# Performance work log

Measured on AMD Instinct MI355X. Metric: run time of the kernel, lower is better.

Reference implementation:

```python
import jax, jax.numpy as jnp
import numpy as np

N_NODES = 1_000_000
N_EDGES = 16_000_000
D = 2          # num_dimensions (hard-coded in source)
H = 64         # hidden_channnels
G = 1024       # number of graphs in the batch


def setup_inputs() -> dict:
    key = jax.random.key(0)
    ks = jax.random.split(key, 10)
    x = jax.random.normal(ks[0], (N_NODES, D), dtype=jnp.float32)
    edge_index = jax.random.randint(ks[1], (2, N_EDGES), 0, N_NODES, dtype=jnp.int64)
    batch = jnp.sort(jax.random.randint(ks[2], (N_NODES,), 0, G, dtype=jnp.int64))
    s = 0.5
    return {
        "x": x,
        "lin_w": jax.random.normal(ks[3], (D, D), dtype=jnp.float32) * s,
        "lin_b": jnp.zeros((D,), jnp.float32),
        "gn_weight": jnp.ones((D,), jnp.float32),
        "gn_bias": jnp.zeros((D,), jnp.float32),
        "gn_mean_scale": jnp.ones((D,), jnp.float32),
        "gcn_w": jax.random.normal(ks[4], (D, D), dtype=jnp.float32) * s,
        "gcn_b": jnp.zeros((D,), jnp.float32),
        "fc1_w": jax.random.normal(ks[5], (H, D), dtype=jnp.float32) * s,
        "fc1_b": jnp.zeros((H,), jnp.float32),
        "fc2_w": jax.random.normal(ks[6], (D, H), dtype=jnp.float32) * (1.0 / np.sqrt(H)),
        "fc2_b": jnp.zeros((D,), jnp.float32),
        "edge_index": edge_index,
        "batch": batch,
    }


def reference(x, lin_w, lin_b, gn_weight, gn_bias, gn_mean_scale,
              gcn_w, gcn_b, fc1_w, fc1_b, fc2_w, fc2_b, edge_index, batch):
    n = x.shape[0]
    # lin
    h = x @ lin_w.T + lin_b
    # GraphNorm called without batch -> single-graph stats; eps = num_dimensions = 2 (arg-order quirk)
    mean = h.mean(axis=0)
    out = h - mean * gn_mean_scale
    var = (out * out).mean(axis=0)
    h = gn_weight * out * jax.lax.rsqrt(var + jnp.float32(D)) + gn_bias
    h = jax.nn.relu(h)
    # GCNConv (add_self_loops=True, sym norm) + residual
    row, col = edge_index[0], edge_index[1]
    deg = jax.ops.segment_sum(jnp.ones_like(col, dtype=h.dtype), col, num_segments=n) + 1.0
    dis = jax.lax.rsqrt(deg)                       # deg^{-1/2}
    hw = h @ gcn_w.T                               # [N, D]
    msg = (dis[row] * dis[col])[:, None] * hw[row] # [E, D]
    agg = jax.ops.segment_sum(msg, col, num_segments=n)
    conv = agg + hw / deg[:, None] + gcn_b         # self-loop term = dis_i^2 * hw_i
    h = conv + h
    # fc1
    h = h @ fc1_w.T + fc1_b                        # [N, H]
    # InstanceNorm1d on 2D input -> unbatched (C=N, L=H): per-row norm over H; eps = H (arg-order quirk)
    m = h.mean(axis=1, keepdims=True)
    v = ((h - m) ** 2).mean(axis=1, keepdims=True)
    h = (h - m) * jax.lax.rsqrt(v + jnp.float32(H))
    # fc2
    h = h @ fc2_w.T + fc2_b                        # [N, D]
    # scatter_mean over batch
    ssum = jax.ops.segment_sum(h, batch, num_segments=G)
    cnt = jax.ops.segment_sum(jnp.ones((n,), h.dtype), batch, num_segments=G)
    return ssum / jnp.maximum(cnt, 1.0)[:, None]
```

## Files before the change

kernel.cpp:

```cpp
#include <hip/hip_runtime.h>

#define BLK 256
#define CH 8192
#define BSHIFT 12
#define BRANGE 4096
#define BMASK 4095
#define NSB 512


__global__ void k_stats(const float* __restrict__ x, int n, double* __restrict__ partials) {
    float s0 = 0.f, s1 = 0.f, s2 = 0.f, s3 = 0.f, s4 = 0.f;
    int nv = n >> 1;
    int stride = gridDim.x * blockDim.x;
    for (int i = blockIdx.x * blockDim.x + threadIdx.x; i < nv; i += stride) {
        float4 v = reinterpret_cast<const float4*>(x)[i];
        s0 += v.x + v.z; s1 += v.y + v.w;
        s2 += v.x * v.x + v.z * v.z;
        s3 += v.y * v.y + v.w * v.w;
        s4 += v.x * v.y + v.z * v.w;
    }
    if (blockIdx.x == 0 && threadIdx.x == 0 && (n & 1)) {
        float2 v = reinterpret_cast<const float2*>(x)[n - 1];
        s0 += v.x; s1 += v.y; s2 += v.x * v.x; s3 += v.y * v.y; s4 += v.x * v.y;
    }
    for (int off = 32; off; off >>= 1) {
        s0 += __shfl_down(s0, off);
        s1 += __shfl_down(s1, off);
        s2 += __shfl_down(s2, off);
        s3 += __shfl_down(s3, off);
        s4 += __shfl_down(s4, off);
    }
    __shared__ double lds[4][5];
    int wid = threadIdx.x >> 6;
    if ((threadIdx.x & 63) == 0) {
        lds[wid][0] = s0; lds[wid][1] = s1; lds[wid][2] = s2;
        lds[wid][3] = s3; lds[wid][4] = s4;
    }
    __syncthreads();
    if (threadIdx.x == 0) {
        double t0 = 0, t1 = 0, t2 = 0, t3 = 0, t4 = 0;
        for (int w = 0; w < 4; ++w) {
            t0 += lds[w][0]; t1 += lds[w][1]; t2 += lds[w][2];
            t3 += lds[w][3]; t4 += lds[w][4];
        }
        double* o = partials + (size_t)blockIdx.x * 5;
        o[0] = t0; o[1] = t1; o[2] = t2; o[3] = t3; o[4] = t4;
    }
}


__global__ void k_params(const double* __restrict__ partials, int np,
                         const int* __restrict__ bhist, int NB,
                         int* __restrict__ gbase, int* __restrict__ cursor,
                         const float* lin_w, const float* lin_b,
                         const float* gn_w, const float* gn_b, const float* gn_ms,
                         const float* gcn_w, const float* gcn_b,
                         const float* fc1_w, const float* fc1_b,
                         const float* fc2_w, const float* fc2_b,
                         int n, float* __restrict__ P) {
    int tid = threadIdx.x;
    if (bhist) {
        __shared__ int si[256];
        int hv = (tid < NB) ? bhist[tid] : 0;
        si[tid] = hv; __syncthreads();
        for (int off = 1; off < 256; off <<= 1) {
            int t = (tid >= off) ? si[tid - off] : 0;
            __syncthreads();
            si[tid] += t;
            __syncthreads();
        }
        if (tid < NB) { gbase[tid] = si[tid] - hv; cursor[tid] = si[tid] - hv; }
        if (tid == 0) gbase[NB] = si[255];
        __syncthreads();
    }
    double a0 = 0, a1 = 0, a2 = 0, a3 = 0, a4 = 0;
    for (int i = tid; i < np; i += blockDim.x) {
        const double* q = partials + (size_t)i * 5;
        a0 += q[0]; a1 += q[1]; a2 += q[2]; a3 += q[3]; a4 += q[4];
    }
    for (int off = 32; off; off >>= 1) {
        a0 += __shfl_down(a0, off);
        a1 += __shfl_down(a1, off);
        a2 += __shfl_down(a2, off);
        a3 += __shfl_down(a3, off);
        a4 += __shfl_down(a4, off);
    }
    __shared__ double red[4][5];
    int wid = tid >> 6;
    if ((tid & 63) == 0) {
        red[wid][0] = a0; red[wid][1] = a1; red[wid][2] = a2;
        red[wid][3] = a3; red[wid][4] = a4;
    }
    __syncthreads();
    if (tid != 0) return;
    double Sx0 = 0, Sx1 = 0, Sxx = 0, Syy = 0, Sxy = 0;
    for (int w = 0; w < 4; ++w) {
        Sx0 += red[w][0]; Sx1 += red[w][1]; Sxx += red[w][2];
        Syy += red[w][3]; Sxy += red[w][4];
    }
    double N = (double)n;
    for (int c = 0; c < 2; ++c) {
        double L0 = lin_w[c * 2], L1 = lin_w[c * 2 + 1], lb = lin_b[c];
        double m   = (L0 * Sx0 + L1 * Sx1) / N + lb;
        double Eh2 = (L0 * L0 * Sxx + L1 * L1 * Syy + 2.0 * L0 * L1 * Sxy
                      + 2.0 * lb * (L0 * Sx0 + L1 * Sx1)) / N + lb * lb;
        double s   = gn_ms[c];
        double var = Eh2 - 2.0 * s * m * m + s * s * m * m;
        double inv = 1.0 / sqrt(var + 2.0);
        double gam = gn_w[c];
        P[c * 2 + 0] = (float)(gam * inv * L0);
        P[c * 2 + 1] = (float)(gam * inv * L1);
        P[4 + c]     = (float)(gam * inv * (lb - m * s) + gn_b[c]);
    }
    P[6] = gcn_w[0]; P[7] = gcn_w[1]; P[8] = gcn_w[2]; P[9] = gcn_w[3];
    P[10] = gcn_b[0]; P[11] = gcn_b[1];
    double b0 = 0, b1 = 0, bb = 0;
    for (int j = 0; j < 64; ++j) { b0 += fc1_w[2 * j]; b1 += fc1_w[2 * j + 1]; bb += fc1_b[j]; }
    b0 /= 64.0; b1 /= 64.0; bb /= 64.0;
    double S00 = 0, S01 = 0, S11 = 0, Sb0 = 0, Sb1 = 0, Sbb = 0;
    double M00 = 0, M01 = 0, M10 = 0, M11 = 0, t0 = 0, t1 = 0;
    for (int j = 0; j < 64; ++j) {
        double w0 = fc1_w[2 * j] - b0, w1 = fc1_w[2 * j + 1] - b1, b = fc1_b[j] - bb;
        S00 += w0 * w0; S01 += w0 * w1; S11 += w1 * w1;
        Sb0 += w0 * b;  Sb1 += w1 * b;  Sbb += b * b;
        double f0 = fc2_w[j], f1 = fc2_w[64 + j];
        M00 += f0 * w0; M01 += f0 * w1; t0 += f0 * b;
        M10 += f1 * w0; M11 += f1 * w1; t1 += f1 * b;
    }
    P[12] = (float)(S00 / 64.0); P[13] = (float)(S01 / 64.0); P[14] = (float)(S11 / 64.0);
    P[15] = (float)(Sb0 / 64.0); P[16] = (float)(Sb1 / 64.0); P[17] = (float)(Sbb / 64.0);
    P[18] = (float)M00; P[19] = (float)M01; P[20] = (float)M10; P[21] = (float)M11;
    P[22] = (float)t0;  P[23] = (float)t1;
    P[24] = fc2_b[0];   P[25] = fc2_b[1];
}


__global__ void k_hist(const int* __restrict__ col, int E, int NB, int* __restrict__ bhist) {
    __shared__ int h[256];
    for (int j = threadIdx.x; j < 256; j += blockDim.x) h[j] = 0;
    __syncthreads();
    int nq = E >> 2;
    int stride = gridDim.x * blockDim.x;
    for (int q = blockIdx.x * blockDim.x + threadIdx.x; q < nq; q += stride) {
        int4 c = reinterpret_cast<const int4*>(col)[q];
        atomicAdd(&h[c.x >> BSHIFT], 1);
        atomicAdd(&h[c.y >> BSHIFT], 1);
        atomicAdd(&h[c.z >> BSHIFT], 1);
        atomicAdd(&h[c.w >> BSHIFT], 1);
    }
    if (blockIdx.x == 0) {
        for (int e = (nq << 2) + threadIdx.x; e < E; e += blockDim.x)
            atomicAdd(&h[col[e] >> BSHIFT], 1);
    }
    __syncthreads();
    for (int j = threadIdx.x; j < NB; j += blockDim.x)
        if (h[j]) atomicAdd(&bhist[j], h[j]);
}

__global__ __launch_bounds__(256) void k_binA(const int* __restrict__ row,
                                              const int* __restrict__ col, int E,
                                              int NB, int* __restrict__ cursor,
                                              unsigned* __restrict__ staging) {
    __shared__ unsigned buf[CH];
    __shared__ int h[256], si[256], lpos[256], lcur[256];
    int tid = threadIdx.x;
    int start = blockIdx.x * CH;
    int end = start + CH; if (end > E) end = E;
    h[tid] = 0;
    __syncthreads();
    for (int e = start + tid; e < end; e += 256)
        atomicAdd(&h[col[e] >> BSHIFT], 1);
    __syncthreads();
    int hv = h[tid];
    si[tid] = hv; __syncthreads();
    for (int off = 1; off < 256; off <<= 1) {
        int t = (tid >= off) ? si[tid - off] : 0;
        __syncthreads();
        si[tid] += t;
        __syncthreads();
    }
    lpos[tid] = si[tid] - hv;
    lcur[tid] = (tid < NB && hv) ? atomicAdd(&cursor[tid], hv) : 0;
    __syncthreads();
    for (int e = start + tid; e < end; e += 256) {
        int c = col[e];
        unsigned w = ((unsigned)row[e] << BSHIFT) | (unsigned)(c & BMASK);
        int slot = atomicAdd(&lpos[c >> BSHIFT], 1);
        buf[slot] = w;
    }
    __syncthreads();
    int wid = tid >> 6, lane = tid & 63;
    for (int b = wid; b < NB; b += 4) {
        int m = h[b];
        if (!m) continue;
        int lb = si[b] - m;
        int g = lcur[b];
        for (int k = lane; k < m; k += 64)
            staging[g + k] = buf[lb + k];
    }
}

__global__ __launch_bounds__(1024) void k_degprep(const unsigned* __restrict__ staging,
                                                  const int* __restrict__ gbase,
                                                  const float* __restrict__ x,
                                                  const float* __restrict__ P,
                                                  int n, int* __restrict__ deg,
                                                  float2* __restrict__ p) {
    __shared__ int hist[BRANGE];
    int tid = threadIdx.x;
    for (int j = tid; j < BRANGE; j += 1024) hist[j] = 0;
    __syncthreads();
    int s = gbase[blockIdx.x], e = gbase[blockIdx.x + 1];
    int pre = (4 - (s & 3)) & 3; int cnt = e - s; if (pre > cnt) pre = cnt;
    for (int i = s + tid; i < s + pre; i += 1024)
        atomicAdd(&hist[staging[i] & BMASK], 1);
    int vs = s + pre;
    int nq = (e - vs) >> 2;
    const uint4* sv = reinterpret_cast<const uint4*>(staging + vs);
    for (int q = tid; q < nq; q += 1024) {
        uint4 w = sv[q];
        atomicAdd(&hist[w.x & BMASK], 1);
        atomicAdd(&hist[w.y & BMASK], 1);
        atomicAdd(&hist[w.z & BMASK], 1);
        atomicAdd(&hist[w.w & BMASK], 1);
    }
    for (int i = vs + (nq << 2) + tid; i < e; i += 1024)
        atomicAdd(&hist[staging[i] & BMASK], 1);
    __syncthreads();
    float A00 = P[0], A01 = P[1], A10 = P[2], A11 = P[3], q0 = P[4], q1 = P[5];
    float g00 = P[6], g01 = P[7], g10 = P[8], g11 = P[9];
    int nb = blockIdx.x << BSHIFT;
    int lim = n - nb; if (lim > BRANGE) lim = BRANGE;
    for (int j = tid; j < lim; j += 1024) {
        int d = hist[j];
        deg[nb + j] = d;
        float2 v = reinterpret_cast<const float2*>(x)[nb + j];
        float gg0 = fmaxf(fmaf(A00, v.x, fmaf(A01, v.y, q0)), 0.f);
        float gg1 = fmaxf(fmaf(A10, v.x, fmaf(A11, v.y, q1)), 0.f);
        float hw0 = g00 * gg0 + g01 * gg1;
        float hw1 = g10 * gg0 + g11 * gg1;
        float degf = (float)d + 1.0f;
        float dis = rsqrtf(degf);
        p[nb + j] = make_float2(dis * hw0, dis * hw1);
    }
}

__global__ void k_aggB(const unsigned* __restrict__ staging, const int* __restrict__ gbase,
                       const float2* __restrict__ p, int n, float2* __restrict__ agg) {
    __shared__ float acc[2 * BRANGE];
    for (int j = threadIdx.x; j < 2 * BRANGE; j += blockDim.x) acc[j] = 0.f;
    __syncthreads();
    int s = gbase[blockIdx.x], e = gbase[blockIdx.x + 1];
    int cnt = e - s;
    int pre = (4 - (s & 3)) & 3; if (pre > cnt) pre = cnt;
    for (int i = s + threadIdx.x; i < s + pre; i += blockDim.x) {
        unsigned w = staging[i]; float2 pv = p[w >> BSHIFT];
        atomicAdd(&acc[2 * (w & BMASK)],     pv.x);
        atomicAdd(&acc[2 * (w & BMASK) + 1], pv.y);
    }
    int vs = s + pre;
    int nq = (e - vs) >> 2;
    const uint4* sv = reinterpret_cast<const uint4*>(staging + vs);
    #pragma unroll 4
    for (int q = threadIdx.x; q < nq; q += blockDim.x) {
        uint4 w = sv[q];
        float2 p0 = p[w.x >> BSHIFT], p1 = p[w.y >> BSHIFT];
        float2 p2 = p[w.z >> BSHIFT], p3 = p[w.w >> BSHIFT];
        atomicAdd(&acc[2 * (w.x & BMASK)],     p0.x);
        atomicAdd(&acc[2 * (w.x & BMASK) + 1], p0.y);
        atomicAdd(&acc[2 * (w.y & BMASK)],     p1.x);
        atomicAdd(&acc[2 * (w.y & BMASK) + 1], p1.y);
        atomicAdd(&acc[2 * (w.z & BMASK)],     p2.x);
        atomicAdd(&acc[2 * (w.z & BMASK) + 1], p2.y);
        atomicAdd(&acc[2 * (w.w & BMASK)],     p3.x);
        atomicAdd(&acc[2 * (w.w & BMASK) + 1], p3.y);
    }
    for (int i = vs + (nq << 2) + threadIdx.x; i < e; i += blockDim.x) {
        unsigned w = staging[i]; float2 pv = p[w >> BSHIFT];
        atomicAdd(&acc[2 * (w & BMASK)],     pv.x);
        atomicAdd(&acc[2 * (w & BMASK) + 1], pv.y);
    }
    __syncthreads();
    int nb = blockIdx.x << BSHIFT;
    for (int j = threadIdx.x; j < BRANGE && nb + j < n; j += blockDim.x)
        agg[nb + j] = make_float2(acc[2 * j], acc[2 * j + 1]);
}


__global__ void k_final(const float* __restrict__ x, const int* __restrict__ deg,
                        const float* __restrict__ agg, const int* __restrict__ batch,
                        const float* __restrict__ P, int n,
                        float* __restrict__ gsum, float* __restrict__ gcnt) {
    int i = blockIdx.x * blockDim.x + threadIdx.x;
    bool valid = i < n;
    float A00 = P[0], A01 = P[1], A10 = P[2], A11 = P[3], q0 = P[4], q1 = P[5];
    float g00 = P[6], g01 = P[7], g10 = P[8], g11 = P[9];
    float gb0 = P[10], gb1 = P[11];
    float S00 = P[12], S01 = P[13], S11 = P[14], Sb0 = P[15], Sb1 = P[16], Sbb = P[17];
    float M00 = P[18], M01 = P[19], M10 = P[20], M11 = P[21];
    float t0 = P[22], t1 = P[23], fb0 = P[24], fb1 = P[25];

    float o0 = 0.f, o1 = 0.f;
    int b = 0;
    if (valid) {
        float2 v = reinterpret_cast<const float2*>(x)[i];
        float g0 = fmaxf(fmaf(A00, v.x, fmaf(A01, v.y, q0)), 0.f);
        float g1 = fmaxf(fmaf(A10, v.x, fmaf(A11, v.y, q1)), 0.f);
        float hw0 = g00 * g0 + g01 * g1;
        float hw1 = g10 * g0 + g11 * g1;
        float degf = (float)deg[i] + 1.0f;
        float dis = rsqrtf(degf);
        float a0 = agg[2 * i], a1 = agg[2 * i + 1];
        float c0 = dis * a0 + hw0 / degf + gb0 + g0;
        float c1 = dis * a1 + hw1 / degf + gb1 + g1;
        float vq = S00 * c0 * c0 + 2.f * S01 * c0 * c1 + S11 * c1 * c1
                 + 2.f * Sb0 * c0 + 2.f * Sb1 * c1 + Sbb;
        float inv = rsqrtf(vq + 64.0f);
        o0 = inv * (M00 * c0 + M01 * c1 + t0) + fb0;
        o1 = inv * (M10 * c0 + M11 * c1 + t1) + fb1;
        b = batch[i];
    }
    unsigned long long act = __ballot(valid);
    if (act == ~0ull) {
        int b0 = __shfl(b, 0);
        if (__all(b == b0)) {
            float s0 = o0, s1 = o1;
            for (int off = 32; off; off >>= 1) {
                s0 += __shfl_down(s0, off);
                s1 += __shfl_down(s1, off);
            }
            if ((threadIdx.x & 63) == 0) {
                atomicAdd(&gsum[2 * b0], s0);
                atomicAdd(&gsum[2 * b0 + 1], s1);
                atomicAdd(&gcnt[b0], 64.0f);
            }
        } else {
            atomicAdd(&gsum[2 * b], o0);
            atomicAdd(&gsum[2 * b + 1], o1);
            atomicAdd(&gcnt[b], 1.0f);
        }
    } else if (valid) {
        atomicAdd(&gsum[2 * b], o0);
        atomicAdd(&gsum[2 * b + 1], o1);
        atomicAdd(&gcnt[b], 1.0f);
    }
}

__global__ void k_div(const float* __restrict__ gsum, const float* __restrict__ gcnt,
                      float* __restrict__ out, int G) {
    int g = blockIdx.x * blockDim.x + threadIdx.x;
    if (g < G) {
        float c = fmaxf(gcnt[g], 1.0f);
        out[2 * g]     = gsum[2 * g] / c;
        out[2 * g + 1] = gsum[2 * g + 1] / c;
    }
}


__global__ void k_prep(const float* __restrict__ x, const int* __restrict__ deg,
                       const float* __restrict__ P, int n, float2* __restrict__ p) {
    int stride = gridDim.x * blockDim.x;
    float A00 = P[0], A01 = P[1], A10 = P[2], A11 = P[3], q0 = P[4], q1 = P[5];
    float g00 = P[6], g01 = P[7], g10 = P[8], g11 = P[9];
    for (int i = blockIdx.x * blockDim.x + threadIdx.x; i < n; i += stride) {
        float2 v = reinterpret_cast<const float2*>(x)[i];
        float g0 = fmaxf(fmaf(A00, v.x, fmaf(A01, v.y, q0)), 0.f);
        float g1 = fmaxf(fmaf(A10, v.x, fmaf(A11, v.y, q1)), 0.f);
        float hw0 = g00 * g0 + g01 * g1;
        float hw1 = g10 * g0 + g11 * g1;
        float degf = (float)deg[i] + 1.0f;
        float dis = rsqrtf(degf);
        p[i] = make_float2(dis * hw0, dis * hw1);
    }
}

__global__ void k_deg(const int* __restrict__ col, int E, int* __restrict__ deg) {
    int nq = (E + 3) >> 2;
    int q = blockIdx.x * blockDim.x + threadIdx.x;
    if (q >= nq) return;
    int base = q << 2;
    if (base + 3 < E) {
        int4 c = reinterpret_cast<const int4*>(col)[q];
        atomicAdd(&deg[c.x], 1); atomicAdd(&deg[c.y], 1);
        atomicAdd(&deg[c.z], 1); atomicAdd(&deg[c.w], 1);
    } else {
        for (int e = base; e < E; ++e) atomicAdd(&deg[col[e]], 1);
    }
}

__global__ void k_edge(const int* __restrict__ row, const int* __restrict__ col, int E,
                       const float2* __restrict__ p, float* __restrict__ agg) {
    int nq = (E + 3) >> 2;
    int q = blockIdx.x * blockDim.x + threadIdx.x;
    if (q >= nq) return;
    int base = q << 2;
    if (base + 3 < E) {
        int4 r = reinterpret_cast<const int4*>(row)[q];
        int4 c = reinterpret_cast<const int4*>(col)[q];
        float2 p0 = p[r.x], p1 = p[r.y], p2 = p[r.z], p3 = p[r.w];
        atomicAdd(&agg[2 * c.x], p0.x); atomicAdd(&agg[2 * c.x + 1], p0.y);
        atomicAdd(&agg[2 * c.y], p1.x); atomicAdd(&agg[2 * c.y + 1], p1.y);
        atomicAdd(&agg[2 * c.z], p2.x); atomicAdd(&agg[2 * c.z + 1], p2.y);
        atomicAdd(&agg[2 * c.w], p3.x); atomicAdd(&agg[2 * c.w + 1], p3.y);
    } else {
        for (int e = base; e < E; ++e) {
            float2 pv = p[row[e]];
            atomicAdd(&agg[2 * col[e]], pv.x);
            atomicAdd(&agg[2 * col[e] + 1], pv.y);
        }
    }
}


extern "C" void kernel_launch(void* const* d_in, const int* in_sizes, int n_in,
                              void* d_out, int out_size, void* d_ws, size_t ws_size,
                              hipStream_t stream) {
    const float* x      = (const float*)d_in[0];
    const float* lin_w  = (const float*)d_in[1];
    const float* lin_b  = (const float*)d_in[2];
    const float* gn_w   = (const float*)d_in[3];
    const float* gn_b   = (const float*)d_in[4];
    const float* gn_ms  = (const float*)d_in[5];
    const float* gcn_w  = (const float*)d_in[6];
    const float* gcn_b  = (const float*)d_in[7];
    const float* fc1_w  = (const float*)d_in[8];
    const float* fc1_b  = (const float*)d_in[9];
    const float* fc2_w  = (const float*)d_in[10];
    const float* fc2_b  = (const float*)d_in[11];
    const int*   ei     = (const int*)d_in[12];
    const int*   batch  = (const int*)d_in[13];

    int n = in_sizes[0] / 2;
    int E = in_sizes[12] / 2;
    int G = out_size / 2;
    const int* row = ei;
    const int* col = ei + E;

    char* ws = (char*)d_ws;
    int nb_nodes = (n + BLK - 1) / BLK;

    int NB = (n + BRANGE - 1) >> BSHIFT;

    size_t zero_end  = 16384 + (size_t)12 * G;
    size_t part_off  = (zero_end + 255) & ~(size_t)255;
    size_t deg_off   = (part_off + (size_t)40 * NSB + 255) & ~(size_t)255;
    size_t p_off     = deg_off + (size_t)4 * n;
    size_t agg_off   = p_off + (size_t)8 * n;
    size_t stag_off  = agg_off + (size_t)8 * n;
    size_t need      = stag_off + (size_t)4 * E;

    bool fast = (n <= (1 << 20)) && (NB <= 253) && (need <= ws_size) &&
                (zero_end <= 16384 + 12288);

    if (fast) {
        float*    P       = (float*)(ws + 64);
        int*      bhist   = (int*)(ws + 4096);
        int*      gbase   = (int*)(ws + 8192);
        int*      cursor  = (int*)(ws + 12288);
        float*    gsum    = (float*)(ws + 16384);
        float*    gcnt    = (float*)(ws + 16384 + (size_t)8 * G);
        double*   part    = (double*)(ws + part_off);
        int*      deg     = (int*)(ws + deg_off);
        float2*   p       = (float2*)(ws + p_off);
        float*    agg     = (float*)(ws + agg_off);
        unsigned* staging = (unsigned*)(ws + stag_off);

        hipMemsetAsync(d_ws, 0, zero_end, stream);

        int nbinA = (E + CH - 1) / CH;

        k_stats<<<NSB, BLK, 0, stream>>>(x, n, part);
        k_hist<<<512, BLK, 0, stream>>>(col, E, NB, bhist);
        k_params<<<1, 256, 0, stream>>>(part, NSB, bhist, NB, gbase, cursor,
                                        lin_w, lin_b, gn_w, gn_b, gn_ms,
                                        gcn_w, gcn_b, fc1_w, fc1_b, fc2_w, fc2_b, n, P);
        k_binA<<<nbinA, 256, 0, stream>>>(row, col, E, NB, cursor, staging);
        k_degprep<<<NB, 1024, 0, stream>>>(staging, gbase, x, P, n, deg, p);
        k_aggB<<<NB, 1024, 0, stream>>>(staging, gbase, p, n, (float2*)agg);
        k_final<<<nb_nodes, BLK, 0, stream>>>(x, deg, agg, batch, P, n, gsum, gcnt);
        k_div<<<(G + BLK - 1) / BLK, BLK, 0, stream>>>(gsum, gcnt, (float*)d_out, G);
    } else {
        float*  P     = (float*)(ws + 64);
        float*  gsum  = (float*)(ws + 4096);
        float*  gcnt  = (float*)(ws + 4096 + (size_t)8 * G);
        size_t fzero_end = 4096 + (size_t)12 * G;
        size_t fpart_off = (fzero_end + 255) & ~(size_t)255;
        size_t fdeg_off  = (fpart_off + (size_t)40 * NSB + 255) & ~(size_t)255;
        int*    deg   = (int*)(ws + fdeg_off);
        size_t fagg_off = fdeg_off + (size_t)4 * n;
        float*  agg   = (float*)(ws + fagg_off);
        size_t fp_off = fagg_off + (size_t)8 * n;
        float2* p     = (float2*)(ws + fp_off);
        double* part  = (double*)(ws + fpart_off);

        hipMemsetAsync(ws + 4096, 0, fzero_end - 4096, stream);
        hipMemsetAsync(ws + fdeg_off, 0, (size_t)12 * n, stream);

        int nq = (E + 3) >> 2;
        int nb_edge = (nq + BLK - 1) / BLK;

        k_stats<<<NSB, BLK, 0, stream>>>(x, n, part);
        k_deg<<<nb_edge, BLK, 0, stream>>>(col, E, deg);
        k_params<<<1, 256, 0, stream>>>(part, NSB, (const int*)nullptr, 0,
                                        (int*)nullptr, (int*)nullptr,
                                        lin_w, lin_b, gn_w, gn_b, gn_ms,
                                        gcn_w, gcn_b, fc1_w, fc1_b, fc2_w, fc2_b, n, P);
        k_prep<<<nb_nodes, BLK, 0, stream>>>(x, deg, P, n, p);
        k_edge<<<nb_edge, BLK, 0, stream>>>(row, col, E, p, agg);
        k_final<<<nb_nodes, BLK, 0, stream>>>(x, deg, agg, batch, P, n, gsum, gcnt);
        k_div<<<(G + BLK - 1) / BLK, BLK, 0, stream>>>(gsum, gcnt, (float*)d_out, G);
    }
}
```

Measured before the change: 401.9 us.

## Halve bucket range and fuse aggregation with final per-node epilogue

The destination-bucket width drops from 4096 to 2048 nodes. The per-bucket kernels therefore launch about twice as many 1024-thread blocks, which fills more compute units, and the bucket scans now handle two bins per thread. The shared-memory aggregation kernel is fused with the final per-node computation: it recomputes hw, applies the GCN residual, the instance-norm closed form and fc2, then does the wavefront-reduced scatter-mean atomics. This removes the agg buffer's global write and read and one kernel launch. In exchange the fused kernel has more register pressure and repeats a little per-node arithmetic.

```diff
diff --git a/kernel.cpp b/kernel.cpp
--- a/kernel.cpp
+++ b/kernel.cpp
@@ -2,9 +2,9 @@
 
 #define BLK 256
 #define CH 8192
-#define BSHIFT 12
-#define BRANGE 4096
-#define BMASK 4095
+#define BSHIFT 11
+#define BRANGE 2048
+#define BMASK 2047
 #define NSB 512
 
 
@@ -61,16 +61,19 @@
     int tid = threadIdx.x;
     if (bhist) {
         __shared__ int si[256];
-        int hv = (tid < NB) ? bhist[tid] : 0;
-        si[tid] = hv; __syncthreads();
+        int v0 = (2 * tid     < NB) ? bhist[2 * tid]     : 0;
+        int v1 = (2 * tid + 1 < NB) ? bhist[2 * tid + 1] : 0;
+        si[tid] = v0 + v1; __syncthreads();
         for (int off = 1; off < 256; off <<= 1) {
             int t = (tid >= off) ? si[tid - off] : 0;
             __syncthreads();
             si[tid] += t;
             __syncthreads();
         }
-        if (tid < NB) { gbase[tid] = si[tid] - hv; cursor[tid] = si[tid] - hv; }
-        if (tid == 0) gbase[NB] = si[255];
+        int base = si[tid] - v0 - v1;
+        if (2 * tid < NB)     { gbase[2 * tid]     = base;      cursor[2 * tid]     = base; }
+        if (2 * tid + 1 < NB) { gbase[2 * tid + 1] = base + v0; cursor[2 * tid + 1] = base + v0; }
+        if (tid == 255) gbase[NB] = si[255];
         __syncthreads();
     }
     double a0 = 0, a1 = 0, a2 = 0, a3 = 0, a4 = 0;
@@ -136,8 +139,8 @@
 
 
 __global__ void k_hist(const int* __restrict__ col, int E, int NB, int* __restrict__ bhist) {
-    __shared__ int h[256];
-    for (int j = threadIdx.x; j < 256; j += blockDim.x) h[j] = 0;
+    __shared__ int h[512];
+    for (int j = threadIdx.x; j < 512; j += blockDim.x) h[j] = 0;
     __syncthreads();
     int nq = E >> 2;
     int stride = gridDim.x * blockDim.x;
@@ -162,25 +165,29 @@
                                               int NB, int* __restrict__ cursor,
                                               unsigned* __restrict__ staging) {
     __shared__ unsigned buf[CH];
-    __shared__ int h[256], si[256], lpos[256], lcur[256];
+    __shared__ int h[512], lpos[512], lcur[512];
+    __shared__ int si[256];
     int tid = threadIdx.x;
     int start = blockIdx.x * CH;
     int end = start + CH; if (end > E) end = E;
-    h[tid] = 0;
+    h[tid] = 0; h[tid + 256] = 0;
     __syncthreads();
     for (int e = start + tid; e < end; e += 256)
         atomicAdd(&h[col[e] >> BSHIFT], 1);
     __syncthreads();
-    int hv = h[tid];
-    si[tid] = hv; __syncthreads();
+    int v0 = h[2 * tid], v1 = h[2 * tid + 1];
+    si[tid] = v0 + v1; __syncthreads();
     for (int off = 1; off < 256; off <<= 1) {
         int t = (tid >= off) ? si[tid - off] : 0;
         __syncthreads();
         si[tid] += t;
         __syncthreads();
     }
-    lpos[tid] = si[tid] - hv;
-    lcur[tid] = (tid < NB && hv) ? atomicAdd(&cursor[tid], hv) : 0;
+    int base = si[tid] - v0 - v1;
+    lpos[2 * tid]     = base;
+    lpos[2 * tid + 1] = base + v0;
+    lcur[2 * tid]     = (2 * tid     < NB && v0) ? atomicAdd(&cursor[2 * tid],     v0) : 0;
+    lcur[2 * tid + 1] = (2 * tid + 1 < NB && v1) ? atomicAdd(&cursor[2 * tid + 1], v1) : 0;
     __syncthreads();
     for (int e = start + tid; e < end; e += 256) {
         int c = col[e];
@@ -193,7 +200,7 @@
     for (int b = wid; b < NB; b += 4) {
         int m = h[b];
         if (!m) continue;
-        int lb = si[b] - m;
+        int lb = lpos[b] - m;
         int g = lcur[b];
         for (int k = lane; k < m; k += 64)
             staging[g + k] = buf[lb + k];
@@ -245,15 +252,20 @@
     }
 }
 
-__global__ void k_aggB(const unsigned* __restrict__ staging, const int* __restrict__ gbase,
-                       const float2* __restrict__ p, int n, float2* __restrict__ agg) {
+__global__ __launch_bounds__(1024) void k_aggfin(
+        const unsigned* __restrict__ staging, const int* __restrict__ gbase,
+        const float2* __restrict__ p, const float* __restrict__ x,
+        const int* __restrict__ deg, const int* __restrict__ batch,
+        const float* __restrict__ Pp, int n,
+        float* __restrict__ gsum, float* __restrict__ gcnt) {
     __shared__ float acc[2 * BRANGE];
-    for (int j = threadIdx.x; j < 2 * BRANGE; j += blockDim.x) acc[j] = 0.f;
+    int tid = threadIdx.x;
+    for (int j = tid; j < 2 * BRANGE; j += 1024) acc[j] = 0.f;
     __syncthreads();
     int s = gbase[blockIdx.x], e = gbase[blockIdx.x + 1];
     int cnt = e - s;
     int pre = (4 - (s & 3)) & 3; if (pre > cnt) pre = cnt;
-    for (int i = s + threadIdx.x; i < s + pre; i += blockDim.x) {
+    for (int i = s + tid; i < s + pre; i += 1024) {
         unsigned w = staging[i]; float2 pv = p[w >> BSHIFT];
         atomicAdd(&acc[2 * (w & BMASK)],     pv.x);
         atomicAdd(&acc[2 * (w & BMASK) + 1], pv.y);
@@ -262,7 +274,7 @@
     int nq = (e - vs) >> 2;
     const uint4* sv = reinterpret_cast<const uint4*>(staging + vs);
     #pragma unroll 4
-    for (int q = threadIdx.x; q < nq; q += blockDim.x) {
+    for (int q = tid; q < nq; q += 1024) {
         uint4 w = sv[q];
         float2 p0 = p[w.x >> BSHIFT], p1 = p[w.y >> BSHIFT];
         float2 p2 = p[w.z >> BSHIFT], p3 = p[w.w >> BSHIFT];
@@ -275,17 +287,130 @@
         atomicAdd(&acc[2 * (w.w & BMASK)],     p3.x);
         atomicAdd(&acc[2 * (w.w & BMASK) + 1], p3.y);
     }
-    for (int i = vs + (nq << 2) + threadIdx.x; i < e; i += blockDim.x) {
+    for (int i = vs + (nq << 2) + tid; i < e; i += 1024) {
         unsigned w = staging[i]; float2 pv = p[w >> BSHIFT];
         atomicAdd(&acc[2 * (w & BMASK)],     pv.x);
         atomicAdd(&acc[2 * (w & BMASK) + 1], pv.y);
     }
     __syncthreads();
+
+    float A00 = Pp[0], A01 = Pp[1], A10 = Pp[2], A11 = Pp[3], q0f = Pp[4], q1f = Pp[5];
+    float g00 = Pp[6], g01 = Pp[7], g10 = Pp[8], g11 = Pp[9];
+    float gb0 = Pp[10], gb1 = Pp[11];
+    float S00 = Pp[12], S01 = Pp[13], S11 = Pp[14], Sb0 = Pp[15], Sb1 = Pp[16], Sbb = Pp[17];
+    float M00 = Pp[18], M01 = Pp[19], M10 = Pp[20], M11 = Pp[21];
+    float t0 = Pp[22], t1 = Pp[23], fb0 = Pp[24], fb1 = Pp[25];
     int nb = blockIdx.x << BSHIFT;
-    for (int j = threadIdx.x; j < BRANGE && nb + j < n; j += blockDim.x)
-        agg[nb + j] = make_float2(acc[2 * j], acc[2 * j + 1]);
-}
-
+    int lim = n - nb; if (lim > BRANGE) lim = BRANGE;
+    for (int j = tid; j < lim; j += 1024) {
+        int i = nb + j;
+        float2 v = reinterpret_cast<const float2*>(x)[i];
+        float g0 = fmaxf(fmaf(A00, v.x, fmaf(A01, v.y, q0f)), 0.f);
+        float g1 = fmaxf(fmaf(A10, v.x, fmaf(A11, v.y, q1f)), 0.f);
+        float hw0 = g00 * g0 + g01 * g1;
+        float hw1 = g10 * g0 + g11 * g1;
+        float degf = (float)deg[i] + 1.0f;
+        float dis = rsqrtf(degf);
+        float a0v = acc[2 * j], a1v = acc[2 * j + 1];
+        float c0 = dis * a0v + hw0 / degf + gb0 + g0;
+        float c1 = dis * a1v + hw1 / degf + gb1 + g1;
+        float vq = S00 * c0 * c0 + 2.f * S01 * c0 * c1 + S11 * c1 * c1
+                 + 2.f * Sb0 * c0 + 2.f * Sb1 * c1 + Sbb;
+        float inv = rsqrtf(vq + 64.0f);
+        float o0 = inv * (M00 * c0 + M01 * c1 + t0) + fb0;
+        float o1 = inv * (M10 * c0 + M11 * c1 + t1) + fb1;
+        int bg = batch[i];
+        unsigned long long act = __ballot(true);
+        if (act == ~0ull) {
+            int b0 = __shfl(bg, 0);
+            if (__all(bg == b0)) {
+                float s0 = o0, s1 = o1;
+                for (int off = 32; off; off >>= 1) {
+                    s0 += __shfl_down(s0, off);
+                    s1 += __shfl_down(s1, off);
+                }
+                if ((tid & 63) == 0) {
+                    atomicAdd(&gsum[2 * b0], s0);
+                    atomicAdd(&gsum[2 * b0 + 1], s1);
+                    atomicAdd(&gcnt[b0], 64.0f);
+                }
+            } else {
+                atomicAdd(&gsum[2 * bg], o0);
+                atomicAdd(&gsum[2 * bg + 1], o1);
+                atomicAdd(&gcnt[bg], 1.0f);
+            }
+        } else {
+            atomicAdd(&gsum[2 * bg], o0);
+            atomicAdd(&gsum[2 * bg + 1], o1);
+            atomicAdd(&gcnt[bg], 1.0f);
+        }
+    }
+}
+
+__global__ void k_div(const float* __restrict__ gsum, const float* __restrict__ gcnt,
+                      float* __restrict__ out, int G) {
+    int g = blockIdx.x * blockDim.x + threadIdx.x;
+    if (g < G) {
+        float c = fmaxf(gcnt[g], 1.0f);
+        out[2 * g]     = gsum[2 * g] / c;
+        out[2 * g + 1] = gsum[2 * g + 1] / c;
+    }
+}
+
+
+__global__ void k_prep(const float* __restrict__ x, const int* __restrict__ deg,
+                       const float* __restrict__ P, int n, float2* __restrict__ p) {
+    int stride = gridDim.x * blockDim.x;
+    float A00 = P[0], A01 = P[1], A10 = P[2], A11 = P[3], q0 = P[4], q1 = P[5];
+    float g00 = P[6], g01 = P[7], g10 = P[8], g11 = P[9];
+    for (int i = blockIdx.x * blockDim.x + threadIdx.x; i < n; i += stride) {
+        float2 v = reinterpret_cast<const float2*>(x)[i];
+        float g0 = fmaxf(fmaf(A00, v.x, fmaf(A01, v.y, q0)), 0.f);
+        float g1 = fmaxf(fmaf(A10, v.x, fmaf(A11, v.y, q1)), 0.f);
+        float hw0 = g00 * g0 + g01 * g1;
+        float hw1 = g10 * g0 + g11 * g1;
+        float degf = (float)deg[i] + 1.0f;
+        float dis = rsqrtf(degf);
+        p[i] = make_float2(dis * hw0, dis * hw1);
+    }
+}
+
+__global__ void k_deg(const int* __restrict__ col, int E, int* __restrict__ deg) {
+    int nq = (E + 3) >> 2;
+    int q = blockIdx.x * blockDim.x + threadIdx.x;
+    if (q >= nq) return;
+    int base = q << 2;
+    if (base + 3 < E) {
+        int4 c = reinterpret_cast<const int4*>(col)[q];
+        atomicAdd(&deg[c.x], 1); atomicAdd(&deg[c.y], 1);
+        atomicAdd(&deg[c.z], 1); atomicAdd(&deg[c.w], 1);
+    } else {
+        for (int e = base; e < E; ++e) atomicAdd(&deg[col[e]], 1);
+    }
+}
+
+__global__ void k_edge(const int* __restrict__ row, const int* __restrict__ col, int E,
+                       const float2* __restrict__ p, float* __restrict__ agg) {
+    int nq = (E + 3) >> 2;
+    int q = blockIdx.x * blockDim.x + threadIdx.x;
+    if (q >= nq) return;
+    int base = q << 2;
+    if (base + 3 < E) {
+        int4 r = reinterpret_cast<const int4*>(row)[q];
+        int4 c = reinterpret_cast<const int4*>(col)[q];
+        float2 p0 = p[r.x], p1 = p[r.y], p2 = p[r.z], p3 = p[r.w];
+        atomicAdd(&agg[2 * c.x], p0.x); atomicAdd(&agg[2 * c.x + 1], p0.y);
+        atomicAdd(&agg[2 * c.y], p1.x); atomicAdd(&agg[2 * c.y + 1], p1.y);
+        atomicAdd(&agg[2 * c.z], p2.x); atomicAdd(&agg[2 * c.z + 1], p2.y);
+        atomicAdd(&agg[2 * c.w], p3.x); atomicAdd(&agg[2 * c.w + 1], p3.y);
+    } else {
+        for (int e = base; e < E; ++e) {
+            float2 pv = p[row[e]];
+            atomicAdd(&agg[2 * col[e]], pv.x);
+            atomicAdd(&agg[2 * col[e] + 1], pv.y);
+        }
+    }
+}
 
 __global__ void k_final(const float* __restrict__ x, const int* __restrict__ deg,
                         const float* __restrict__ agg, const int* __restrict__ batch,
@@ -346,71 +471,6 @@
     }
 }
 
-__global__ void k_div(const float* __restrict__ gsum, const float* __restrict__ gcnt,
-                      float* __restrict__ out, int G) {
-    int g = blockIdx.x * blockDim.x + threadIdx.x;
-    if (g < G) {
-        float c = fmaxf(gcnt[g], 1.0f);
-        out[2 * g]     = gsum[2 * g] / c;
-        out[2 * g + 1] = gsum[2 * g + 1] / c;
-    }
-}
-
-
-__global__ void k_prep(const float* __restrict__ x, const int* __restrict__ deg,
-                       const float* __restrict__ P, int n, float2* __restrict__ p) {
-    int stride = gridDim.x * blockDim.x;
-    float A00 = P[0], A01 = P[1], A10 = P[2], A11 = P[3], q0 = P[4], q1 = P[5];
-    float g00 = P[6], g01 = P[7], g10 = P[8], g11 = P[9];
-    for (int i = blockIdx.x * blockDim.x + threadIdx.x; i < n; i += stride) {
-        float2 v = reinterpret_cast<const float2*>(x)[i];
-        float g0 = fmaxf(fmaf(A00, v.x, fmaf(A01, v.y, q0)), 0.f);
-        float g1 = fmaxf(fmaf(A10, v.x, fmaf(A11, v.y, q1)), 0.f);
-        float hw0 = g00 * g0 + g01 * g1;
-        float hw1 = g10 * g0 + g11 * g1;
-        float degf = (float)deg[i] + 1.0f;
-        float dis = rsqrtf(degf);
-        p[i] = make_float2(dis * hw0, dis * hw1);
-    }
-}
-
-__global__ void k_deg(const int* __restrict__ col, int E, int* __restrict__ deg) {
-    int nq = (E + 3) >> 2;
-    int q = blockIdx.x * blockDim.x + threadIdx.x;
-    if (q >= nq) return;
-    int base = q << 2;
-    if (base + 3 < E) {
-        int4 c = reinterpret_cast<const int4*>(col)[q];
-        atomicAdd(&deg[c.x], 1); atomicAdd(&deg[c.y], 1);
-        atomicAdd(&deg[c.z], 1); atomicAdd(&deg[c.w], 1);
-    } else {
-        for (int e = base; e < E; ++e) atomicAdd(&deg[col[e]], 1);
-    }
-}
-
-__global__ void k_edge(const int* __restrict__ row, const int* __restrict__ col, int E,
-                       const float2* __restrict__ p, float* __restrict__ agg) {
-    int nq = (E + 3) >> 2;
-    int q = blockIdx.x * blockDim.x + threadIdx.x;
-    if (q >= nq) return;
-    int base = q << 2;
-    if (base + 3 < E) {
-        int4 r = reinterpret_cast<const int4*>(row)[q];
-        int4 c = reinterpret_cast<const int4*>(col)[q];
-        float2 p0 = p[r.x], p1 = p[r.y], p2 = p[r.z], p3 = p[r.w];
-        atomicAdd(&agg[2 * c.x], p0.x); atomicAdd(&agg[2 * c.x + 1], p0.y);
-        atomicAdd(&agg[2 * c.y], p1.x); atomicAdd(&agg[2 * c.y + 1], p1.y);
-        atomicAdd(&agg[2 * c.z], p2.x); atomicAdd(&agg[2 * c.z + 1], p2.y);
-        atomicAdd(&agg[2 * c.w], p3.x); atomicAdd(&agg[2 * c.w + 1], p3.y);
-    } else {
-        for (int e = base; e < E; ++e) {
-            float2 pv = p[row[e]];
-            atomicAdd(&agg[2 * col[e]], pv.x);
-            atomicAdd(&agg[2 * col[e] + 1], pv.y);
-        }
-    }
-}
-
 
 extern "C" void kernel_launch(void* const* d_in, const int* in_sizes, int n_in,
                               void* d_out, int out_size, void* d_ws, size_t ws_size,
@@ -438,18 +498,16 @@
 
     char* ws = (char*)d_ws;
     int nb_nodes = (n + BLK - 1) / BLK;
-
     int NB = (n + BRANGE - 1) >> BSHIFT;
 
     size_t zero_end  = 16384 + (size_t)12 * G;
     size_t part_off  = (zero_end + 255) & ~(size_t)255;
     size_t deg_off   = (part_off + (size_t)40 * NSB + 255) & ~(size_t)255;
     size_t p_off     = deg_off + (size_t)4 * n;
-    size_t agg_off   = p_off + (size_t)8 * n;
-    size_t stag_off  = agg_off + (size_t)8 * n;
+    size_t stag_off  = p_off + (size_t)8 * n;
     size_t need      = stag_off + (size_t)4 * E;
 
-    bool fast = (n <= (1 << 20)) && (NB <= 253) && (need <= ws_size) &&
+    bool fast = (n <= (1 << 20)) && (NB <= 511) && (need <= ws_size) &&
                 (zero_end <= 16384 + 12288);
 
     if (fast) {
@@ -462,7 +520,6 @@
         double*   part    = (double*)(ws + part_off);
         int*      deg     = (int*)(ws + deg_off);
         float2*   p       = (float2*)(ws + p_off);
-        float*    agg     = (float*)(ws + agg_off);
         unsigned* staging = (unsigned*)(ws + stag_off);
 
         hipMemsetAsync(d_ws, 0, zero_end, stream);
@@ -476,8 +533,8 @@
                                         gcn_w, gcn_b, fc1_w, fc1_b, fc2_w, fc2_b, n, P);
         k_binA<<<nbinA, 256, 0, stream>>>(row, col, E, NB, cursor, staging);
         k_degprep<<<NB, 1024, 0, stream>>>(staging, gbase, x, P, n, deg, p);
-        k_aggB<<<NB, 1024, 0, stream>>>(staging, gbase, p, n, (float2*)agg);
-        k_final<<<nb_nodes, BLK, 0, stream>>>(x, deg, agg, batch, P, n, gsum, gcnt);
+        k_aggfin<<<NB, 1024, 0, stream>>>(staging, gbase, p, x, deg, batch,
+                                          P, n, gsum, gcnt);
         k_div<<<(G + BLK - 1) / BLK, BLK, 0, stream>>>(gsum, gcnt, (float*)d_out, G);
     } else {
         float*  P     = (float*)(ws + 64);
```

Result: slower. 441.4 us (+9.8%).
